# Optimization experiments

Hardware: AMD Instinct MI355X
Metric: run time of the kernel (lower is better)

## Reference

```python
import jax, jax.numpy as jnp
import numpy as np

B, IN, OUT, Q = 2048, 1024, 1024, 16

def setup_inputs() -> dict:
    key = jax.random.key(0)
    k1, k2, k3, k4 = jax.random.split(key, 4)
    bound = 1.0 / np.sqrt(IN)
    x = jax.random.normal(k1, (B, IN), dtype=jnp.float32)
    indices = jax.random.randint(k2, (B, IN), 0, Q, dtype=jnp.int32)
    # param_index: per-(quantile, input-feature) weight vector of length size_out
    param_table = jax.random.uniform(k3, (Q, IN, OUT), dtype=jnp.float32,
                                     minval=-bound, maxval=bound)
    bias = jax.random.uniform(k4, (OUT,), dtype=jnp.float32,
                              minval=-bound, maxval=bound)
    return {"x": x, "indices": indices, "param_table": param_table,
            "bias": bias, "store_activations": 0, "get_indices": 0, "use_db": 0}

def reference(x, indices, param_table, bias, store_activations, get_indices, use_db):
    # out[b, o] = sum_i param_table[indices[b,i], i, o] * x[b,i]  + bias[o]
    # Expressed as Q masked matmuls to avoid a [B, IN, OUT] gathered intermediate:
    # route each (b, i) contribution to its quantile's weight slab.
    q = param_table.shape[0]
    onehot = jax.nn.one_hot(indices, q, dtype=x.dtype)      # [B, IN, Q]
    xq = onehot * x[..., None]                               # [B, IN, Q]
    w_times_x = jnp.einsum('biq,qio->bo', xq, param_table)   # [B, OUT]
    return w_times_x + bias
```

## Files before the change

### kernel.cpp

```cpp
#include <hip/hip_runtime.h>
#include <stdint.h>

#define B_SZ   2048
#define IN_SZ  1024
#define OUT_SZ 1024
#define Q_SZ   16
#define NZB    4

typedef __attribute__((ext_vector_type(8))) short short8;
typedef __attribute__((ext_vector_type(4))) float floatx4;
typedef __attribute__((ext_vector_type(2))) unsigned short u16x2;
typedef __attribute__((ext_vector_type(2))) short s16x2;

__device__ __forceinline__ unsigned short f32_to_bf16_rne(float f) {
    union { float f; uint32_t u; } v; v.f = f;
    uint32_t u = v.u;
    return (unsigned short)((u + 0x7FFFu + ((u >> 16) & 1u)) >> 16);
}

__device__ __forceinline__ uint32_t mask3(uint32_t xv, uint32_t ohv, unsigned short sh) {
    union { uint32_t u; u16x2 v; s16x2 s; } t;
    t.u = ohv;
    u16x2 shv; shv.x = sh; shv.y = sh;
    t.v = t.v << shv;
    s16x2 f15; f15.x = 15; f15.y = 15;
    t.s = t.s >> f15;
    return xv & t.u;
}

__global__ void k_build_wf(const float* __restrict__ W, unsigned short* __restrict__ Wf) {
    const int S = blockIdx.x;
    const int q = S & 15, ih = (S >> 4) & 3, xb = (S >> 6) & 7, zb = S >> 9;
    const int t = threadIdx.x;
    const int i0 = zb * 256 + ih * 64;
    const int o0 = xb * 128;
    __shared__ unsigned short lds[64][130];

#pragma unroll
    for (int it = 0; it < 8; ++it) {
        int r  = it * 8 + (t >> 5);
        int c4 = (t & 31) * 4;
        float4 v = *(const float4*)(W + ((size_t)(q * 1024 + i0 + r)) * 1024 + o0 + c4);
        unsigned short h0 = f32_to_bf16_rne(v.x), h1 = f32_to_bf16_rne(v.y);
        unsigned short h2 = f32_to_bf16_rne(v.z), h3 = f32_to_bf16_rne(v.w);
        *(uint32_t*)&lds[r][c4]     = (uint32_t)h0 | ((uint32_t)h1 << 16);
        *(uint32_t*)&lds[r][c4 + 2] = (uint32_t)h2 | ((uint32_t)h3 << 16);
    }
    __syncthreads();

    unsigned short* dst = Wf + (size_t)S * 8192;
#pragma unroll
    for (int it = 0; it < 4; ++it) {
        int c = it * 256 + t;
        int L = c & 63;
        int hnt = c >> 6;
        int h = hnt >> 3, nt = hnt & 7;
        int ol = nt * 16 + (L & 15);
        int il = h * 32 + (L >> 4) * 8;
        unsigned short v[8];
#pragma unroll
        for (int j = 0; j < 8; ++j) v[j] = lds[il + j][ol];
        *(uint4*)(dst + (size_t)c * 8) = *(uint4*)v;
    }
}

__global__ __launch_bounds__(256, 2) void k_gemm(const unsigned short* __restrict__ Wf,
                                                 const float* __restrict__ x,
                                                 const int* __restrict__ idx,
                                                 float* __restrict__ P) {
    const int tid  = threadIdx.x;
    const int wave = tid >> 6, lane = tid & 63;

    const int id = blockIdx.x;
    const int zb = id & 3;
    const int xb = (id >> 2) & 7;
    const int yb = id >> 5;
    const int o0 = xb * 128, b0 = yb * 128, ibase = zb * 256;

    const char* wbase = (const char*)Wf + (size_t)(zb * 8 + xb) * 64 * 16384;
    const int   lofs  = lane * 16;

    const int arow = b0 + wave * 32 + (lane & 15);
    const float* xg = x + (size_t)arow * IN_SZ + ibase + (lane >> 4) * 8;
    const int*   ig = idx + (size_t)arow * IN_SZ + ibase + (lane >> 4) * 8;

    floatx4 acc[16];
#pragma unroll
    for (int i = 0; i < 16; ++i) acc[i] = (floatx4){0.f, 0.f, 0.f, 0.f};

    uint4 xr[2][2], oh[2][2];
    short8 rb0[8], rb1[8], rb2[8], rb3[8];

#define LOADB(d, s, h)                                                        \
    {   const char* p_ = wbase + (size_t)(s) * 16384 + (h) * 8192 + lofs;     \
        _Pragma("unroll")                                                     \
        for (int nt_ = 0; nt_ < 8; ++nt_)                                     \
            (d)[nt_] = *(const short8*)(p_ + nt_ * 1024);                     \
    }

#define RELOADA(ih)                                                           \
    {   int io_ = (ih) * 64;                                                  \
        _Pragma("unroll")                                                     \
        for (int mt_ = 0; mt_ < 2; ++mt_)                                     \
            _Pragma("unroll")                                                 \
            for (int hh_ = 0; hh_ < 2; ++hh_) {                               \
                const float* xp_ = xg + mt_ * 16 * IN_SZ + io_ + hh_ * 32;    \
                const int*   ip_ = ig + mt_ * 16 * IN_SZ + io_ + hh_ * 32;    \
                float a_[8]; int b_[8];                                       \
                *(float4*)(a_)     = *(const float4*)xp_;                     \
                *(float4*)(a_ + 4) = *((const float4*)xp_ + 1);               \
                *(int4*)(b_)       = *(const int4*)ip_;                       \
                *(int4*)(b_ + 4)   = *((const int4*)ip_ + 1);                 \
                unsigned short xv_[8];                                        \
                _Pragma("unroll")                                             \
                for (int j_ = 0; j_ < 8; ++j_) xv_[j_] = f32_to_bf16_rne(a_[j_]); \
                xr[mt_][hh_] = *(uint4*)xv_;                                  \
                uint32_t iw_[4];                                              \
                _Pragma("unroll")                                             \
                for (int w_ = 0; w_ < 4; ++w_)                                \
                    iw_[w_] = (1u << b_[2 * w_]) | ((1u << b_[2 * w_ + 1]) << 16); \
                oh[mt_][hh_] = *(uint4*)iw_;                                  \
            }                                                                 \
    }

#define MASKS(hh)                                                             \
        _Pragma("unroll")                                                     \
        for (int mt_ = 0; mt_ < 2; ++mt_) {                                   \
            aF[mt_].u.x = mask3(xr[mt_][hh].x, oh[mt_][hh].x, sh_);           \
            aF[mt_].u.y = mask3(xr[mt_][hh].y, oh[mt_][hh].y, sh_);           \
            aF[mt_].u.z = mask3(xr[mt_][hh].z, oh[mt_][hh].z, sh_);           \
            aF[mt_].u.w = mask3(xr[mt_][hh].w, oh[mt_][hh].w, sh_);           \
        }

#define SLAB(s_, Bc0, Bc1, Bn0, Bn1)                                          \
    {   if ((s_) && (((s_) & 15) == 0)) RELOADA((s_) >> 4);                   \
        if ((s_) < 63) LOADB(Bn0, (s_) + 1, 0);                               \
        const unsigned short sh_ = (unsigned short)(15 - ((s_) & 15));        \
        union { uint4 u; short8 s8; } aF[2];                                  \
        MASKS(0);                                                             \
        _Pragma("unroll")                                                     \
        for (int mt_ = 0; mt_ < 2; ++mt_)                                     \
            _Pragma("unroll")                                                 \
            for (int nt_ = 0; nt_ < 8; ++nt_)                                 \
                acc[mt_ * 8 + nt_] = __builtin_amdgcn_mfma_f32_16x16x32_bf16( \
                    aF[mt_].s8, (Bc0)[nt_], acc[mt_ * 8 + nt_], 0, 0, 0);     \
        if ((s_) < 63) LOADB(Bn1, (s_) + 1, 1);                               \
        MASKS(1);                                                             \
        _Pragma("unroll")                                                     \
        for (int mt_ = 0; mt_ < 2; ++mt_)                                     \
            _Pragma("unroll")                                                 \
            for (int nt_ = 0; nt_ < 8; ++nt_)                                 \
                acc[mt_ * 8 + nt_] = __builtin_amdgcn_mfma_f32_16x16x32_bf16( \
                    aF[mt_].s8, (Bc1)[nt_], acc[mt_ * 8 + nt_], 0, 0, 0);     \
    }

    RELOADA(0);
    LOADB(rb0, 0, 0);
    LOADB(rb1, 0, 1);

#pragma unroll 1
    for (int g = 0; g < 32; ++g) {
        SLAB(2 * g,     rb0, rb1, rb2, rb3);
        SLAB(2 * g + 1, rb2, rb3, rb0, rb1);
    }

    float* Pz = P + (size_t)zb * (B_SZ * OUT_SZ);
    int cn = lane & 15, rq = lane >> 4;
#pragma unroll
    for (int mt = 0; mt < 2; ++mt)
#pragma unroll
        for (int nt = 0; nt < 8; ++nt) {
            int bb = b0 + wave * 32 + mt * 16 + rq * 4;
            int oo = o0 + nt * 16 + cn;
#pragma unroll
            for (int e = 0; e < 4; ++e)
                Pz[(size_t)(bb + e) * OUT_SZ + oo] = acc[mt * 8 + nt][e];
        }
#undef LOADB
#undef RELOADA
#undef MASKS
#undef SLAB
}

__global__ void k_reduce(const float* __restrict__ P, const float* __restrict__ bias,
                         float* __restrict__ out) {
    int t = blockIdx.x * 256 + threadIdx.x;
    const float4* b4 = (const float4*)bias;
    float4 a = b4[t & 255];
#pragma unroll
    for (int z = 0; z < NZB; ++z) {
        float4 v = ((const float4*)P)[(size_t)z * (B_SZ * OUT_SZ / 4) + t];
        a.x += v.x; a.y += v.y; a.z += v.z; a.w += v.w;
    }
    ((float4*)out)[t] = a;
}

__global__ void k_naive(const float* __restrict__ x, const int* __restrict__ idx,
                        const float* __restrict__ W, const float* __restrict__ bias,
                        float* __restrict__ out) {
    int b = blockIdx.x;
    int o = threadIdx.x * 4;
    float4 acc = *(const float4*)(bias + o);
    const float* xr = x + (size_t)b * IN_SZ;
    const int*   ir = idx + (size_t)b * IN_SZ;
    for (int i = 0; i < IN_SZ; ++i) {
        float xv = xr[i];
        int q = ir[i];
        float4 w4 = *(const float4*)(W + ((size_t)q * IN_SZ + i) * OUT_SZ + o);
        acc.x += xv * w4.x; acc.y += xv * w4.y;
        acc.z += xv * w4.z; acc.w += xv * w4.w;
    }
    *(float4*)(out + (size_t)b * OUT_SZ + o) = acc;
}

extern "C" void kernel_launch(void* const* d_in, const int* in_sizes, int n_in,
                              void* d_out, int out_size, void* d_ws, size_t ws_size,
                              hipStream_t stream) {
    const float* x    = (const float*)d_in[0];
    const int*   idx  = (const int*)d_in[1];
    const float* W    = (const float*)d_in[2];
    const float* bias = (const float*)d_in[3];
    float* out = (float*)d_out;

    const size_t wf_bytes = (size_t)2048 * 16384;
    const size_t p_bytes  = (size_t)NZB * B_SZ * OUT_SZ * 4;
    if (ws_size < wf_bytes + p_bytes) {
        k_naive<<<dim3(B_SZ), dim3(256), 0, stream>>>(x, idx, W, bias, out);
        return;
    }
    unsigned short* Wf = (unsigned short*)d_ws;
    float* P = (float*)((char*)d_ws + wf_bytes);

    k_build_wf<<<dim3(2048), dim3(256), 0, stream>>>(W, Wf);
    k_gemm<<<dim3(NZB * 8 * (B_SZ / 128)), dim3(256), 0, stream>>>(Wf, x, idx, P);
    k_reduce<<<dim3(2048), dim3(256), 0, stream>>>(P, bias, out);
}
```

Before: 205.7 us.

## Stage shared weight slabs through LDS with async global-to-LDS loads

Before this change, every wave loaded the full bf16 weight slab from global memory into its own registers, so the four waves of a block fetched the same data four times. Now the waves cooperatively copy each 16 KB slab into a double-buffered LDS area using global_load_lds, each wave handling a quarter. MFMA B fragments are then read from LDS. This cuts redundant global/L2 traffic and frees the large register prefetch buffers. The cost is 32 KB of LDS per block, an extra LDS read pass and a block-wide barrier per slab, and correctness depends on the async LDS writes being complete at that barrier.

```diff
diff --git a/kernel.cpp b/kernel.cpp
--- a/kernel.cpp
+++ b/kernel.cpp
@@ -28,6 +28,12 @@
     return xv & t.u;
 }
 
+__device__ __forceinline__ void gload_lds16(const void* g, void* l) {
+    __builtin_amdgcn_global_load_lds(
+        (const __attribute__((address_space(1))) unsigned int*)g,
+        (__attribute__((address_space(3))) unsigned int*)l, 16, 0, 0);
+}
+
 __global__ void k_build_wf(const float* __restrict__ W, unsigned short* __restrict__ Wf) {
     const int S = blockIdx.x;
     const int q = S & 15, ih = (S >> 4) & 3, xb = (S >> 6) & 7, zb = S >> 9;
@@ -80,6 +86,8 @@
     const char* wbase = (const char*)Wf + (size_t)(zb * 8 + xb) * 64 * 16384;
     const int   lofs  = lane * 16;
 
+    __shared__ unsigned char sm[2][16384];
+
     const int arow = b0 + wave * 32 + (lane & 15);
     const float* xg = x + (size_t)arow * IN_SZ + ibase + (lane >> 4) * 8;
     const int*   ig = idx + (size_t)arow * IN_SZ + ibase + (lane >> 4) * 8;
@@ -89,14 +97,6 @@
     for (int i = 0; i < 16; ++i) acc[i] = (floatx4){0.f, 0.f, 0.f, 0.f};
 
     uint4 xr[2][2], oh[2][2];
-    short8 rb0[8], rb1[8], rb2[8], rb3[8];
-
-#define LOADB(d, s, h)                                                        \
-    {   const char* p_ = wbase + (size_t)(s) * 16384 + (h) * 8192 + lofs;     \
-        _Pragma("unroll")                                                     \
-        for (int nt_ = 0; nt_ < 8; ++nt_)                                     \
-            (d)[nt_] = *(const short8*)(p_ + nt_ * 1024);                     \
-    }
 
 #define RELOADA(ih)                                                           \
     {   int io_ = (ih) * 64;                                                  \
@@ -132,36 +132,53 @@
             aF[mt_].u.w = mask3(xr[mt_][hh].w, oh[mt_][hh].w, sh_);           \
         }
 
-#define SLAB(s_, Bc0, Bc1, Bn0, Bn1)                                          \
-    {   if ((s_) && (((s_) & 15) == 0)) RELOADA((s_) >> 4);                   \
-        if ((s_) < 63) LOADB(Bn0, (s_) + 1, 0);                               \
+    const int soff = wave * 4096 + lofs;
+#define STAGE(s_, pb_)                                                        \
+    {   const char* gp_ = wbase + (size_t)(s_) * 16384 + soff;                \
+        unsigned char* lp_ = &sm[pb_][soff];                                  \
+        gload_lds16(gp_,        lp_);                                         \
+        gload_lds16(gp_ + 1024, lp_ + 1024);                                  \
+        gload_lds16(gp_ + 2048, lp_ + 2048);                                  \
+        gload_lds16(gp_ + 3072, lp_ + 3072);                                  \
+    }
+
+#define SLAB(s_, pc_, pn_)                                                    \
+    {   if ((s_) < 63) STAGE((s_) + 1, pn_);                                  \
+        if ((s_) && (((s_) & 15) == 0)) RELOADA((s_) >> 4);                   \
         const unsigned short sh_ = (unsigned short)(15 - ((s_) & 15));        \
         union { uint4 u; short8 s8; } aF[2];                                  \
+        short8 f_[8];                                                         \
+        _Pragma("unroll")                                                     \
+        for (int nt_ = 0; nt_ < 8; ++nt_)                                     \
+            f_[nt_] = *(const short8*)&sm[pc_][nt_ * 1024 + lofs];            \
         MASKS(0);                                                             \
         _Pragma("unroll")                                                     \
         for (int mt_ = 0; mt_ < 2; ++mt_)                                     \
             _Pragma("unroll")                                                 \
             for (int nt_ = 0; nt_ < 8; ++nt_)                                 \
                 acc[mt_ * 8 + nt_] = __builtin_amdgcn_mfma_f32_16x16x32_bf16( \
-                    aF[mt_].s8, (Bc0)[nt_], acc[mt_ * 8 + nt_], 0, 0, 0);     \
-        if ((s_) < 63) LOADB(Bn1, (s_) + 1, 1);                               \
+                    aF[mt_].s8, f_[nt_], acc[mt_ * 8 + nt_], 0, 0, 0);        \
+        _Pragma("unroll")                                                     \
+        for (int nt_ = 0; nt_ < 8; ++nt_)                                     \
+            f_[nt_] = *(const short8*)&sm[pc_][8192 + nt_ * 1024 + lofs];     \
         MASKS(1);                                                             \
         _Pragma("unroll")                                                     \
         for (int mt_ = 0; mt_ < 2; ++mt_)                                     \
             _Pragma("unroll")                                                 \
             for (int nt_ = 0; nt_ < 8; ++nt_)                                 \
                 acc[mt_ * 8 + nt_] = __builtin_amdgcn_mfma_f32_16x16x32_bf16( \
-                    aF[mt_].s8, (Bc1)[nt_], acc[mt_ * 8 + nt_], 0, 0, 0);     \
+                    aF[mt_].s8, f_[nt_], acc[mt_ * 8 + nt_], 0, 0, 0);        \
+        __syncthreads();                                                      \
     }
 
     RELOADA(0);
-    LOADB(rb0, 0, 0);
-    LOADB(rb1, 0, 1);
+    STAGE(0, 0);
+    __syncthreads();
 
 #pragma unroll 1
     for (int g = 0; g < 32; ++g) {
-        SLAB(2 * g,     rb0, rb1, rb2, rb3);
-        SLAB(2 * g + 1, rb2, rb3, rb0, rb1);
+        SLAB(2 * g,     0, 1);
+        SLAB(2 * g + 1, 1, 0);
     }
 
     float* Pz = P + (size_t)zb * (B_SZ * OUT_SZ);
@@ -176,9 +193,9 @@
             for (int e = 0; e < 4; ++e)
                 Pz[(size_t)(bb + e) * OUT_SZ + oo] = acc[mt * 8 + nt][e];
         }
-#undef LOADB
 #undef RELOADA
 #undef MASKS
+#undef STAGE
 #undef SLAB
 }
 
```

Result: faster. 192.1 us (-6.6%).
